# Optimization experiments

Hardware: AMD Instinct MI355X
Metric: run time of the kernel (lower is better)

Reference implementation:

```python
import jax, jax.numpy as jnp
import numpy as np

EMBED_DIM = 1024
NUM_HEADS = 16
HEAD_DIM = EMBED_DIM // NUM_HEADS


def setup_inputs() -> dict:
    key = jax.random.key(0)
    ks = jax.random.split(key, 7)
    B, S, E = 2, 2048, EMBED_DIM
    # xavier_uniform bound for square [E, E] weight
    bound = float(np.sqrt(6.0 / (E + E)))
    mkw = lambda k: jax.random.uniform(k, (E, E), jnp.float32, -bound, bound)
    return {
        "query": jax.random.normal(ks[0], (B, S, E), jnp.float32),
        "key": jax.random.normal(ks[1], (B, S, E), jnp.float32),
        "value": jax.random.normal(ks[2], (B, S, E), jnp.float32),
        "Wq": mkw(ks[3]),
        "Wk": mkw(ks[4]),
        "Wv": mkw(ks[5]),
        "Wo": mkw(ks[6]),
    }


def reference(query, key, value, Wq, Wk, Wv, Wo):
    # Chunked sigmoid attention: since sigmoid has no cross-key normalization
    # and all projections are bias-free linear maps, summing per-KV-chunk
    # partial outputs is mathematically identical to the full computation:
    #   out = (sigmoid(scale * Q K^T) @ V) @ Wo^T
    B, L, E = query.shape
    H, D = NUM_HEADS, HEAD_DIM
    scale = D ** -0.5
    q = (query @ Wq.T).reshape(B, L, H, D) * scale   # [B,L,H,D]
    k = (key @ Wk.T).reshape(B, -1, H, D)            # [B,S,H,D]
    v = (value @ Wv.T).reshape(B, -1, H, D)          # [B,S,H,D]
    scores = jax.nn.sigmoid(jnp.einsum('blhd,bshd->bhls', q, k))  # [B,H,L,S]
    o = jnp.einsum('bhls,bshd->blhd', scores, v).reshape(B, L, E)
    return o @ Wo.T
```

## Files before the change

### kernel.cpp

```cpp
#include <hip/hip_runtime.h>

typedef float f32x4 __attribute__((ext_vector_type(4)));
typedef float f32x16 __attribute__((ext_vector_type(16)));
typedef __bf16 bf16x4 __attribute__((ext_vector_type(4)));
typedef __bf16 bf16x8 __attribute__((ext_vector_type(8)));

constexpr int E = 1024;
constexpr int S = 2048;
constexpr int Bsz = 2;
constexpr int H = 16;
constexpr int Dh = 64;
constexpr int M = Bsz * S;
constexpr int E2 = 2048;

#define GLOAD_LDS16(g, l)                                                                 \
  __builtin_amdgcn_global_load_lds((const __attribute__((address_space(1))) void*)(g),    \
                                   (__attribute__((address_space(3))) void*)(l), 16, 0, 0)

__device__ __forceinline__ unsigned pk2(float a, float b) {
  union { __bf16 h[2]; unsigned u; } r;
  r.h[0] = (__bf16)a; r.h[1] = (__bf16)b;
  return r.u;
}

__global__ __launch_bounds__(256) void convert_bf16(
    const float* __restrict__ q, const float* __restrict__ k,
    const float* __restrict__ v, const float* __restrict__ wq,
    const float* __restrict__ wk, const float* __restrict__ wv,
    const float* __restrict__ wo, __bf16* __restrict__ aq,
    __bf16* __restrict__ ak, __bf16* __restrict__ av,
    __bf16* __restrict__ wqkv, __bf16* __restrict__ wob) {
  const int id = blockIdx.y;
  const float* src;
  __bf16* dst;
  int n;
  float scale = 1.0f;
  switch (id) {
    case 0: src = q;  dst = aq;             n = M * E; break;
    case 1: src = k;  dst = ak;             n = M * E; break;
    case 2: src = v;  dst = av;             n = M * E; break;
    case 3: src = wq; dst = wqkv;           n = E * E; scale = -0.18033688f; break;
    case 4: src = wk; dst = wqkv + E * E;   n = E * E; break;
    case 5: src = wv; dst = wqkv + 2 * E * E; n = E * E; break;
    default: src = wo; dst = wob;           n = E * E; break;
  }
  const int stride = gridDim.x * 256 * 8;
  for (int i = (blockIdx.x * 256 + threadIdx.x) * 8; i < n; i += stride) {
    f32x4 a = *reinterpret_cast<const f32x4*>(&src[i]);
    f32x4 b = *reinterpret_cast<const f32x4*>(&src[i + 4]);
    bf16x8 o;
    o[0] = (__bf16)(a[0] * scale); o[1] = (__bf16)(a[1] * scale);
    o[2] = (__bf16)(a[2] * scale); o[3] = (__bf16)(a[3] * scale);
    o[4] = (__bf16)(b[0] * scale); o[5] = (__bf16)(b[1] * scale);
    o[6] = (__bf16)(b[2] * scale); o[7] = (__bf16)(b[3] * scale);
    *reinterpret_cast<bf16x8*>(&dst[i]) = o;
  }
}

__global__ __launch_bounds__(256) void gemm_qkv(
    const __bf16* __restrict__ A0, const __bf16* __restrict__ A1,
    const __bf16* __restrict__ A2, const __bf16* __restrict__ Bw,
    __bf16* __restrict__ C0, __bf16* __restrict__ C1, __bf16* __restrict__ C2) {
  constexpr int NT  = 32;
  constexpr int NTN = 24;
  constexpr int NWG = 32 * NTN;
  constexpr int CPX = NWG / 8;

  __shared__ char smem[2][16384];

  const int t    = threadIdx.x;
  const int lane = t & 63;
  const int wid  = t >> 6;
  const int wr   = (wid >> 1) * 64;
  const int wc   = (wid & 1) * 64;
  const int r16  = lane & 15;
  const int g4   = lane >> 4;

  const int bid = blockIdx.x;
  const int fid = (bid & 7) * CPX + (bid >> 3);
  const int mt  = fid / NTN;
  const int nt  = fid % NTN;
  const int tm  = mt * 128;
  const int tn  = nt * 128;
  const int which = tn >> 10;

  const __bf16* Ab = which == 0 ? A0 : which == 1 ? A1 : A2;

  auto stage = [&](int kt, int buf) {
    const int k0 = kt * 32;
    char* dst = smem[buf];
#pragma unroll
    for (int c = wid; c < 16; c += 4) {
      const bool isA = c < 8;
      const int cc   = isA ? c : c - 8;
      const int row  = cc * 16 + (lane >> 2);
      const int sx   = (lane & 3) ^ ((row >> 1) & 3);
      const __bf16* src = isA ? &Ab[(size_t)(tm + row) * 1024 + k0 + sx * 8]
                              : &Bw[(size_t)(tn + row) * 1024 + k0 + sx * 8];
      GLOAD_LDS16(src, dst + c * 1024);
    }
  };

  stage(0, 0);
  stage(1, 1);

  f32x4 acc[4][4] = {};

  for (int kt = 0; kt < NT; ++kt) {
    const int buf = kt & 1;
    if (kt + 1 < NT) {
      asm volatile("s_waitcnt vmcnt(4)" ::: "memory");
    } else {
      asm volatile("s_waitcnt vmcnt(0)" ::: "memory");
    }
    __builtin_amdgcn_s_barrier();
    __builtin_amdgcn_sched_barrier(0);

    const char* As = smem[buf];
    const char* Bs = smem[buf] + 8192;

    bf16x8 af[4], bfv[4];
#pragma unroll
    for (int mi = 0; mi < 4; ++mi) {
      int row = wr + mi * 16 + r16;
      int g   = g4 ^ ((row >> 1) & 3);
      af[mi] = *reinterpret_cast<const bf16x8*>(As + row * 64 + g * 16);
    }
#pragma unroll
    for (int ni = 0; ni < 4; ++ni) {
      int row = wc + ni * 16 + r16;
      int g   = g4 ^ ((row >> 1) & 3);
      bfv[ni] = *reinterpret_cast<const bf16x8*>(Bs + row * 64 + g * 16);
    }

    __builtin_amdgcn_s_setprio(1);
#pragma unroll
    for (int mi = 0; mi < 4; ++mi)
#pragma unroll
      for (int ni = 0; ni < 4; ++ni)
        acc[mi][ni] = __builtin_amdgcn_mfma_f32_16x16x32_bf16(af[mi], bfv[ni],
                                                              acc[mi][ni], 0, 0, 0);
    __builtin_amdgcn_s_setprio(0);

    __builtin_amdgcn_sched_barrier(0);
    __builtin_amdgcn_s_barrier();
    if (kt + 2 < NT) stage(kt + 2, buf);
  }

#pragma unroll
  for (int mi = 0; mi < 4; ++mi) {
#pragma unroll
    for (int ni = 0; ni < 4; ++ni) {
#pragma unroll
      for (int j = 0; j < 4; ++j) {
        float v = acc[mi][ni][j];
        int m = tm + wr + mi * 16 + ((lane >> 4) << 2) + j;
        int n = tn + wc + ni * 16 + r16;
        int nl = n & 1023;
        int b = m >> 11, s = m & 2047, h = nl >> 6, d = nl & 63;
        __bf16* Cout = which == 0 ? C0 : which == 1 ? C1 : C2;
        if (which < 2) {
          Cout[((size_t)(b * H + h) * S + s) * Dh + d] = (__bf16)v;
        } else {
          int ssw = (s & ~12) | ((s & 4) << 1) | ((s & 8) >> 1);
          Cout[((size_t)(b * H + h) * Dh + d) * S + ssw] = (__bf16)v;
        }
      }
    }
  }
}

template <int TM, int MODE, int KS>
__global__ __launch_bounds__(256) void gemm_bf16nt(
    const __bf16* __restrict__ A0, const __bf16* __restrict__ A1,
    const __bf16* __restrict__ A2, const __bf16* __restrict__ Bw,
    void* __restrict__ C0, void* __restrict__ C1, void* __restrict__ C2) {
  static_assert(TM == 64, "vmcnt literal assumes TM=64 (6 chunks/wave)");
  constexpr int MI  = TM / 32;
  constexpr int NT  = KS / 64;
  constexpr int ACH = TM / 8;
  constexpr int NCH = ACH + 16;
  constexpr int NTN = 8;
  constexpr int NWG = NTN * (M / TM);
  constexpr int CPX = NWG / 8;

  __shared__ char smem[2][NCH * 1024];

  const int t    = threadIdx.x;
  const int lane = t & 63;
  const int wid  = t >> 6;
  const int wr   = (wid >> 1) * (TM / 2);
  const int wc   = (wid & 1) * 64;
  const int r16  = lane & 15;

  const int bid = blockIdx.x;
  const int fid = (bid & 7) * CPX + (bid >> 3);
  const int mt  = fid / NTN;
  const int nt  = fid % NTN;
  const int tm  = mt * TM;
  const int tn  = nt * 128;

  const __bf16* Ab = A0;

  auto stage = [&](int kt, int buf) {
    const int k0  = kt * 64;
    const int k0b = k0 & 1023;
    char* dst = smem[buf];
#pragma unroll
    for (int c = wid; c < NCH; c += 4) {
      const bool isA = c < ACH;
      const int cc   = isA ? c : c - ACH;
      const int L    = cc * 1024 + lane * 16;
      const int row  = L >> 7;
      const int sw   = ((L >> 4) & 7) ^ (row & 7);
      const __bf16* src = isA ? &Ab[(size_t)(tm + row) * KS + k0 + sw * 8]
                              : &Bw[(size_t)(tn + row) * 1024 + k0b + sw * 8];
      GLOAD_LDS16(src, dst + c * 1024);
    }
  };

  stage(0, 0);
  stage(1, 1);

  f32x4 acc[MI][4] = {};

  for (int kt = 0; kt < NT; ++kt) {
    const int buf = kt & 1;
    if (kt + 1 < NT) {
      asm volatile("s_waitcnt vmcnt(6)" ::: "memory");
    } else {
      asm volatile("s_waitcnt vmcnt(0)" ::: "memory");
    }
    __builtin_amdgcn_s_barrier();
    __builtin_amdgcn_sched_barrier(0);

    const __bf16* As = (const __bf16*)smem[buf];
    const __bf16* Bs = (const __bf16*)(smem[buf] + ACH * 1024);

#pragma unroll
    for (int kc = 0; kc < 2; ++kc) {
      bf16x8 af[MI], bfv[4];
#pragma unroll
      for (int mi = 0; mi < MI; ++mi) {
        int row = wr + mi * 16 + r16;
        int g   = (kc * 4 + (lane >> 4)) ^ (row & 7);
        af[mi] = *reinterpret_cast<const bf16x8*>(&As[row * 64 + g * 8]);
      }
#pragma unroll
      for (int ni = 0; ni < 4; ++ni) {
        int row = wc + ni * 16 + r16;
        int g   = (kc * 4 + (lane >> 4)) ^ (row & 7);
        bfv[ni] = *reinterpret_cast<const bf16x8*>(&Bs[row * 64 + g * 8]);
      }
      __builtin_amdgcn_s_setprio(1);
#pragma unroll
      for (int mi = 0; mi < MI; ++mi)
#pragma unroll
        for (int ni = 0; ni < 4; ++ni)
          acc[mi][ni] = __builtin_amdgcn_mfma_f32_16x16x32_bf16(af[mi], bfv[ni],
                                                                acc[mi][ni], 0, 0, 0);
      __builtin_amdgcn_s_setprio(0);
    }

    __builtin_amdgcn_sched_barrier(0);
    __builtin_amdgcn_s_barrier();
    if (kt + 2 < NT) stage(kt + 2, buf);
  }

#pragma unroll
  for (int mi = 0; mi < MI; ++mi) {
#pragma unroll
    for (int ni = 0; ni < 4; ++ni) {
#pragma unroll
      for (int j = 0; j < 4; ++j) {
        float v = acc[mi][ni][j];
        int m = tm + wr + mi * 16 + ((lane >> 4) << 2) + j;
        int n = tn + wc + ni * 16 + r16;
        ((float*)C0)[(size_t)m * E + n] = v;
      }
    }
  }
}

__global__ __launch_bounds__(64, 2) void attn_sigmoid(const __bf16* __restrict__ Q,
                                                      const __bf16* __restrict__ K,
                                                      const __bf16* __restrict__ Vt,
                                                      __bf16* __restrict__ O) {
  __shared__ char smem[16384];

  const int t    = threadIdx.x;
  const int lane = t & 63;
  const int l31  = lane & 31;
  const int hh   = lane >> 5;
  const int qt   = blockIdx.x >> 1;
  const int ss   = blockIdx.x & 1;
  const int q0   = qt * 64;
  const int h    = blockIdx.y;
  const int b    = blockIdx.z;

  const __bf16* Qh = Q + (size_t)(b * H + h) * S * Dh;
  const __bf16* Kh = K + (size_t)(b * H + h) * S * Dh;
  const __bf16* Vh = Vt + (size_t)(b * H + h) * Dh * S;

  const __bf16* kSrc = Kh + (size_t)(ss * 1024 + (lane >> 3)) * Dh +
                       (((lane & 7) ^ (lane >> 3)) * 8);
  const __bf16* vSrc = Vh + (size_t)(lane >> 2) * S + ss * 1024 +
                       (((lane & 3) ^ ((lane >> 3) & 3)) * 8);

  auto stage = [&](int it, int buf) {
    char* dst = smem + buf * 8192;
#pragma unroll
    for (int j = 0; j < 4; ++j)
      GLOAD_LDS16(kSrc + it * 2048 + j * 512, dst + j * 1024);
#pragma unroll
    for (int j = 0; j < 4; ++j)
      GLOAD_LDS16(vSrc + it * 32 + (size_t)j * 16 * S, dst + 4096 + j * 1024);
  };

  bf16x8 Qf[2][4];
#pragma unroll
  for (int g = 0; g < 2; ++g)
#pragma unroll
    for (int kc = 0; kc < 4; ++kc)
      Qf[g][kc] = *reinterpret_cast<const bf16x8*>(
          &Qh[(size_t)(q0 + g * 32 + l31) * Dh + kc * 16 + hh * 8]);

  stage(0, 0);
  stage(1, 1);

  f32x16 ot[2][2] = {};

#pragma unroll 2
  for (int it = 0; it < 32; ++it) {
    const int buf = it & 1;
    if (it + 1 < 32) {
      asm volatile("s_waitcnt vmcnt(8)" ::: "memory");
    } else {
      asm volatile("s_waitcnt vmcnt(0)" ::: "memory");
    }
    __builtin_amdgcn_sched_barrier(0);

    const __bf16* Kb = (const __bf16*)(smem + buf * 8192);
    const __bf16* Vb = (const __bf16*)(smem + buf * 8192 + 4096);

    bf16x8 kf[4], vf[4];
#pragma unroll
    for (int kc = 0; kc < 4; ++kc) {
      int x = (2 * kc + hh) ^ (l31 & 7);
      kf[kc] = *reinterpret_cast<const bf16x8*>(&Kb[l31 * 64 + x * 8]);
    }
#pragma unroll
    for (int kc2 = 0; kc2 < 2; ++kc2)
#pragma unroll
      for (int dblk = 0; dblk < 2; ++dblk) {
        int row = dblk * 32 + l31;
        int x   = (2 * kc2 + hh) ^ ((l31 >> 1) & 3);
        vf[kc2 * 2 + dblk] = *reinterpret_cast<const bf16x8*>(&Vb[row * 32 + x * 8]);
      }
    asm volatile("s_waitcnt lgkmcnt(0)" ::: "memory");
    __builtin_amdgcn_sched_barrier(0);

    if (it + 2 < 32) stage(it + 2, buf);

    f32x16 s0 = {}, s1 = {};
    __builtin_amdgcn_s_setprio(1);
#pragma unroll
    for (int kc = 0; kc < 4; ++kc) {
      s0 = __builtin_amdgcn_mfma_f32_32x32x16_bf16(kf[kc], Qf[0][kc], s0, 0, 0, 0);
      s1 = __builtin_amdgcn_mfma_f32_32x32x16_bf16(kf[kc], Qf[1][kc], s1, 0, 0, 0);
    }
    __builtin_amdgcn_s_setprio(0);

    bf16x8 F[2][2];
#pragma unroll
    for (int g = 0; g < 2; ++g) {
      union { unsigned u[4]; bf16x8 v; } fu[2];
#pragma unroll
      for (int kc2 = 0; kc2 < 2; ++kc2) {
#pragma unroll
        for (int jj = 0; jj < 4; ++jj) {
          float ya = g ? s1[kc2 * 8 + 2 * jj] : s0[kc2 * 8 + 2 * jj];
          float yb = g ? s1[kc2 * 8 + 2 * jj + 1] : s0[kc2 * 8 + 2 * jj + 1];
          float pa = __builtin_amdgcn_rcpf(1.0f + __builtin_amdgcn_exp2f(ya));
          float pb = __builtin_amdgcn_rcpf(1.0f + __builtin_amdgcn_exp2f(yb));
          fu[kc2].u[jj] = pk2(pa, pb);
        }
        F[g][kc2] = fu[kc2].v;
      }
    }

    __builtin_amdgcn_s_setprio(1);
#pragma unroll
    for (int kc2 = 0; kc2 < 2; ++kc2) {
#pragma unroll
      for (int dblk = 0; dblk < 2; ++dblk) {
        ot[0][dblk] = __builtin_amdgcn_mfma_f32_32x32x16_bf16(
            vf[kc2 * 2 + dblk], F[0][kc2], ot[0][dblk], 0, 0, 0);
        ot[1][dblk] = __builtin_amdgcn_mfma_f32_32x32x16_bf16(
            vf[kc2 * 2 + dblk], F[1][kc2], ot[1][dblk], 0, 0, 0);
      }
    }
    __builtin_amdgcn_s_setprio(0);
  }

  __syncthreads();
  __bf16* Os = (__bf16*)smem;
#pragma unroll
  for (int g = 0; g < 2; ++g) {
    int row = g * 32 + l31;
#pragma unroll
    for (int dblk = 0; dblk < 2; ++dblk)
#pragma unroll
      for (int rp = 0; rp < 4; ++rp) {
        int r  = rp * 4;
        int gg = dblk * 4 + rp;
        int by = row * 128 + ((gg ^ (row & 7)) * 16) + hh * 8;
        float a0 = ot[g][dblk][r];
        float a1 = ot[g][dblk][r + 1];
        float a2 = ot[g][dblk][r + 2];
        float a3 = ot[g][dblk][r + 3];
        unsigned long long val =
            (unsigned long long)pk2(a0, a1) | ((unsigned long long)pk2(a2, a3) << 32);
        *reinterpret_cast<unsigned long long*>((char*)Os + by) = val;
      }
  }
  __syncthreads();
#pragma unroll
  for (int i = 0; i < 8; ++i) {
    int c   = i * 64 + t;
    int row = c >> 3;
    int ch  = c & 7;
    bf16x8 v = *reinterpret_cast<const bf16x8*>(
        (char*)Os + row * 128 + ((ch ^ (row & 7)) * 16));
    *reinterpret_cast<bf16x8*>(
        &O[((size_t)(b * S) + q0 + row) * E2 + ss * 1024 + h * Dh + ch * 8]) = v;
  }
}

extern "C" void kernel_launch(void* const* d_in, const int* in_sizes, int n_in,
                              void* d_out, int out_size, void* d_ws, size_t ws_size,
                              hipStream_t stream) {
  const float* query = (const float*)d_in[0];
  const float* key_  = (const float*)d_in[1];
  const float* value = (const float*)d_in[2];
  const float* Wq    = (const float*)d_in[3];
  const float* Wk    = (const float*)d_in[4];
  const float* Wv    = (const float*)d_in[5];
  const float* Wo    = (const float*)d_in[6];

  char* ws = (char*)d_ws;
  __bf16* aq   = (__bf16*)(ws);
  __bf16* ak   = (__bf16*)(ws + ((size_t)8 << 20));
  __bf16* av   = (__bf16*)(ws + ((size_t)16 << 20));
  __bf16* wqkv = (__bf16*)(ws + ((size_t)24 << 20));
  __bf16* wob  = (__bf16*)(ws + ((size_t)30 << 20));
  __bf16* pq   = (__bf16*)(ws + ((size_t)32 << 20));
  __bf16* pk   = (__bf16*)(ws + ((size_t)40 << 20));
  __bf16* pvt  = (__bf16*)(ws + ((size_t)48 << 20));
  __bf16* ob   = (__bf16*)(ws);

  convert_bf16<<<dim3(512, 7), 256, 0, stream>>>(query, key_, value, Wq, Wk, Wv,
                                                 Wo, aq, ak, av, wqkv, wob);

  gemm_qkv<<<768, 256, 0, stream>>>(aq, ak, av, wqkv, pq, pk, pvt);

  attn_sigmoid<<<dim3(S / 32, H, Bsz), 64, 0, stream>>>(pq, pk, pvt, ob);

  gemm_bf16nt<64, 2, 2048><<<512, 256, 0, stream>>>(
      ob, nullptr, nullptr, wob, (float*)d_out, nullptr, nullptr);
}
```

Measured before the change: 135.6 us.

## Switch QKV GEMM to single-buffered 64-wide K tiles; peel first score MFMA

The QKV projection GEMM drops its double-buffered async pipeline with 32-wide K steps. It now uses a single 32KB buffer holding 64-wide K tiles with an 8-way XOR swizzle, wrapped in two __syncthreads per step. This halves the number of K iterations and barriers, but global loads no longer overlap with MFMA work. The attention kernel also peels the first score MFMA so it accumulates into a constant zero rather than a freshly zeroed register.

Result: faster. 132.7 us (-2.1%).

```diff
diff --git a/kernel.cpp b/kernel.cpp
--- a/kernel.cpp
+++ b/kernel.cpp
@@ -61,12 +61,12 @@
     const __bf16* __restrict__ A0, const __bf16* __restrict__ A1,
     const __bf16* __restrict__ A2, const __bf16* __restrict__ Bw,
     __bf16* __restrict__ C0, __bf16* __restrict__ C1, __bf16* __restrict__ C2) {
-  constexpr int NT  = 32;
+  constexpr int NT  = 16;
   constexpr int NTN = 24;
   constexpr int NWG = 32 * NTN;
   constexpr int CPX = NWG / 8;
 
-  __shared__ char smem[2][16384];
+  __shared__ char smem[32768];
 
   const int t    = threadIdx.x;
   const int lane = t & 63;
@@ -74,7 +74,6 @@
   const int wr   = (wid >> 1) * 64;
   const int wc   = (wid & 1) * 64;
   const int r16  = lane & 15;
-  const int g4   = lane >> 4;
 
   const int bid = blockIdx.x;
   const int fid = (bid & 7) * CPX + (bid >> 3);
@@ -86,65 +85,55 @@
 
   const __bf16* Ab = which == 0 ? A0 : which == 1 ? A1 : A2;
 
-  auto stage = [&](int kt, int buf) {
-    const int k0 = kt * 32;
-    char* dst = smem[buf];
-#pragma unroll
-    for (int c = wid; c < 16; c += 4) {
-      const bool isA = c < 8;
-      const int cc   = isA ? c : c - 8;
-      const int row  = cc * 16 + (lane >> 2);
-      const int sx   = (lane & 3) ^ ((row >> 1) & 3);
-      const __bf16* src = isA ? &Ab[(size_t)(tm + row) * 1024 + k0 + sx * 8]
-                              : &Bw[(size_t)(tn + row) * 1024 + k0 + sx * 8];
-      GLOAD_LDS16(src, dst + c * 1024);
+  auto stage = [&](int kt) {
+    const int k0 = kt * 64;
+#pragma unroll
+    for (int c = wid; c < 32; c += 4) {
+      const bool isA = c < 16;
+      const int cc   = isA ? c : c - 16;
+      const int L    = cc * 1024 + lane * 16;
+      const int row  = L >> 7;
+      const int sw   = ((L >> 4) & 7) ^ (row & 7);
+      const __bf16* src = isA ? &Ab[(size_t)(tm + row) * 1024 + k0 + sw * 8]
+                              : &Bw[(size_t)(tn + row) * 1024 + k0 + sw * 8];
+      GLOAD_LDS16(src, smem + c * 1024);
     }
   };
 
-  stage(0, 0);
-  stage(1, 1);
-
   f32x4 acc[4][4] = {};
 
   for (int kt = 0; kt < NT; ++kt) {
-    const int buf = kt & 1;
-    if (kt + 1 < NT) {
-      asm volatile("s_waitcnt vmcnt(4)" ::: "memory");
-    } else {
-      asm volatile("s_waitcnt vmcnt(0)" ::: "memory");
-    }
-    __builtin_amdgcn_s_barrier();
-    __builtin_amdgcn_sched_barrier(0);
-
-    const char* As = smem[buf];
-    const char* Bs = smem[buf] + 8192;
-
-    bf16x8 af[4], bfv[4];
-#pragma unroll
-    for (int mi = 0; mi < 4; ++mi) {
-      int row = wr + mi * 16 + r16;
-      int g   = g4 ^ ((row >> 1) & 3);
-      af[mi] = *reinterpret_cast<const bf16x8*>(As + row * 64 + g * 16);
-    }
-#pragma unroll
-    for (int ni = 0; ni < 4; ++ni) {
-      int row = wc + ni * 16 + r16;
-      int g   = g4 ^ ((row >> 1) & 3);
-      bfv[ni] = *reinterpret_cast<const bf16x8*>(Bs + row * 64 + g * 16);
-    }
-
-    __builtin_amdgcn_s_setprio(1);
-#pragma unroll
-    for (int mi = 0; mi < 4; ++mi)
-#pragma unroll
-      for (int ni = 0; ni < 4; ++ni)
-        acc[mi][ni] = __builtin_amdgcn_mfma_f32_16x16x32_bf16(af[mi], bfv[ni],
-                                                              acc[mi][ni], 0, 0, 0);
-    __builtin_amdgcn_s_setprio(0);
-
-    __builtin_amdgcn_sched_barrier(0);
-    __builtin_amdgcn_s_barrier();
-    if (kt + 2 < NT) stage(kt + 2, buf);
+    __syncthreads();
+    stage(kt);
+    __syncthreads();
+
+    const char* As = smem;
+    const char* Bs = smem + 16384;
+
+#pragma unroll
+    for (int kc = 0; kc < 2; ++kc) {
+      bf16x8 af[4], bfv[4];
+#pragma unroll
+      for (int mi = 0; mi < 4; ++mi) {
+        int row = wr + mi * 16 + r16;
+        int g   = (kc * 4 + (lane >> 4)) ^ (row & 7);
+        af[mi] = *reinterpret_cast<const bf16x8*>(As + row * 128 + g * 16);
+      }
+#pragma unroll
+      for (int ni = 0; ni < 4; ++ni) {
+        int row = wc + ni * 16 + r16;
+        int g   = (kc * 4 + (lane >> 4)) ^ (row & 7);
+        bfv[ni] = *reinterpret_cast<const bf16x8*>(Bs + row * 128 + g * 16);
+      }
+      __builtin_amdgcn_s_setprio(1);
+#pragma unroll
+      for (int mi = 0; mi < 4; ++mi)
+#pragma unroll
+        for (int ni = 0; ni < 4; ++ni)
+          acc[mi][ni] = __builtin_amdgcn_mfma_f32_16x16x32_bf16(af[mi], bfv[ni],
+                                                                acc[mi][ni], 0, 0, 0);
+      __builtin_amdgcn_s_setprio(0);
+    }
   }
 
 #pragma unroll
@@ -328,6 +317,7 @@
   stage(0, 0);
   stage(1, 1);
 
+  const f32x16 ZERO = {};
   f32x16 ot[2][2] = {};
 
 #pragma unroll 2
@@ -362,10 +352,12 @@
 
     if (it + 2 < 32) stage(it + 2, buf);
 
-    f32x16 s0 = {}, s1 = {};
+    f32x16 s0, s1;
     __builtin_amdgcn_s_setprio(1);
-#pragma unroll
-    for (int kc = 0; kc < 4; ++kc) {
+    s0 = __builtin_amdgcn_mfma_f32_32x32x16_bf16(kf[0], Qf[0][0], ZERO, 0, 0, 0);
+    s1 = __builtin_amdgcn_mfma_f32_32x32x16_bf16(kf[0], Qf[1][0], ZERO, 0, 0, 0);
+#pragma unroll
+    for (int kc = 1; kc < 4; ++kc) {
       s0 = __builtin_amdgcn_mfma_f32_32x32x16_bf16(kf[kc], Qf[0][kc], s0, 0, 0, 0);
       s1 = __builtin_amdgcn_mfma_f32_32x32x16_bf16(kf[kc], Qf[1][kc], s1, 0, 0, 0);
     }
```
